# Optimization experiments

Measured on AMD Instinct MI355X. Metric: run time of the kernel, lower is better.

## Reference

```python
import jax, jax.numpy as jnp
import numpy as np

H = 128          # hidden_size
B = 64           # batch of users
T = 20           # current-session length (== max_sess_len)
S = 10           # friend sessions per user (graph degree)
L = 20           # max_sess_len
NUM_ITEMS = 50000
NUM_USERS = 10000
TOPK = 2         # topk in sess_similarity


def gru(x, W_ih, W_hh, b_ih, b_hh):
    """torch nn.GRU (1 layer, batch_first). x: [N, T, H] -> outputs [N, T, H], h_T [N, H]."""
    h0 = jnp.zeros((x.shape[0], x.shape[-1]), x.dtype)

    def step(h, xt):
        gi = xt @ W_ih.T + b_ih          # [N, 3H]
        gh = h @ W_hh.T + b_hh
        i_r, i_z, i_n = jnp.split(gi, 3, axis=-1)
        h_r, h_z, h_n = jnp.split(gh, 3, axis=-1)
        r = jax.nn.sigmoid(i_r + h_r)
        z = jax.nn.sigmoid(i_z + h_z)
        n = jnp.tanh(i_n + r * h_n)
        h = (1.0 - z) * n + z * h
        return h, h

    hT, ys = jax.lax.scan(step, h0, jnp.swapaxes(x, 0, 1))
    return jnp.swapaxes(ys, 0, 1), hT


def masked_softmax(x, mask, axis):
    neg = jnp.finfo(x.dtype).min
    return jax.nn.softmax(jnp.where(mask, x, neg), axis=axis)


def setup_inputs() -> dict:
    key = jax.random.key(0)
    ks = jax.random.split(key, 12)
    users = jax.random.randint(ks[0], (B,), 0, NUM_USERS)
    cur_sess = jax.random.randint(ks[1], (B, T), 0, NUM_ITEMS)          # all valid -> full length
    hist_sess = jax.random.randint(ks[2], (B, S, L), 0, NUM_ITEMS)
    frds_sess = jax.random.randint(ks[3], (B, S, L), 0, NUM_ITEMS)
    cur_sess_len = jnp.full((B,), T, dtype=jnp.int32)
    # parameters
    v_emb = jax.random.uniform(ks[4], (NUM_ITEMS + 1, H), minval=-1.0, maxval=1.0)
    v_emb = v_emb.at[NUM_ITEMS].set(0.0)                                 # padding_idx row
    u_emb = jax.random.normal(ks[5], (NUM_USERS, H)) * (1.0 / np.sqrt(H))
    sc = 1.0 / np.sqrt(H)
    W_ih = jax.random.normal(ks[6], (3 * H, H)) * sc
    W_hh = jax.random.normal(ks[7], (3 * H, H)) * sc
    b_ih = jnp.zeros((3 * H,), jnp.float32)
    b_hh = jnp.zeros((3 * H,), jnp.float32)
    out1_w = jax.random.normal(ks[8], (NUM_ITEMS, 3 * H)) * (1.0 / np.sqrt(3 * H))
    out1_b = jnp.zeros((NUM_ITEMS,), jnp.float32)
    return dict(users=users, cur_sess=cur_sess, hist_sess=hist_sess, frds_sess=frds_sess,
                cur_sess_len=cur_sess_len, v_emb=v_emb, u_emb=u_emb,
                W_ih=W_ih, W_hh=W_hh, b_ih=b_ih, b_hh=b_hh, out1_w=out1_w, out1_b=out1_b)


def reference(users, cur_sess, hist_sess, frds_sess, cur_sess_len,
              v_emb, u_emb, W_ih, W_hh, b_ih, b_hh, out1_w, out1_b):
    # --- rnn_encoder on current session (dropout p=0, eval) ---
    hs, _ = gru(v_emb[cur_sess], W_ih, W_hh, b_ih, b_hh)                 # [B, T, H]
    query = hs

    # --- friend branch (hist branch is dead: hu is overwritten with zeros) ---
    # sess_encoder: GRU over each friend session's items
    frd_items = v_emb[frds_sess]                                         # [B, S, L, H]
    enc, _ = gru(frd_items.reshape(B * S, L, H), W_ih, W_hh, b_ih, b_hh)
    enc = enc.reshape(B, S, L, H)                                        # encoder_output

    # sess_similarity: max over session positions, softmax over degree (S)
    scores = jnp.einsum('bth,bslh->bstl', query, enc)                    # [B, S, T, L]
    sim_raw = scores.max(axis=-1)                                        # [B, S, T]
    sim1 = jax.nn.softmax(sim_raw, axis=1)
    # preserve: edges that are top-2 most similar for ANY step t (S > TOPK branch)
    _, idx = jax.lax.top_k(jnp.swapaxes(sim1, 1, 2), TOPK)               # [B, T, 2]
    preserve = jax.nn.one_hot(idx, S, dtype=jnp.float32).sum((1, 2)) > 0 # [B, S]

    # sess_embedding_attn on the filtered subgraph (masking == filtering here)
    user_e = u_emb[users]                                                # [B, H]
    w = jax.nn.softmax(jnp.einsum('bh,bslh->bsl', user_e, frd_items), axis=2)
    sess_emb = jnp.einsum('bsl,bslh->bsh', w, frd_items)                 # [B, S, H]

    # user_sess_reduce_func: sim1 (pre-filter softmax values), then two softmaxes
    # over the surviving edges (masked softmax over S)
    m = preserve[:, :, None]                                             # [B, S, 1]
    s = masked_softmax(sim1, m, axis=1)
    s = masked_softmax(s, m, axis=1)
    s = jnp.where(m, s, 0.0)
    hf = jnp.einsum('bst,bsh->bth', s, sess_emb)                         # [B, T, H]

    hu = jnp.zeros_like(hs)                                              # hu = zeros_like(hs)
    output = jnp.concatenate([hs, hu, hf], axis=-1)                      # [B, T, 3H]
    logits = output @ out1_w.T + out1_b                                  # [B, T, NUM_ITEMS]
    return logits
```

## Files before the change

kernel.cpp:

```cpp
#include <hip/hip_runtime.h>
#include <cstdint>
#include <cstddef>

#define H_      128
#define B_      64
#define T_      20
#define S_      10
#define L_      20
#define NITEMS  50000
#define NSEQ    704
#define NTOK    (NSEQ * 20)
#define NPAD    50048
#define KA      256

typedef __attribute__((ext_vector_type(8))) short short8;
typedef __attribute__((ext_vector_type(4))) float f32x4;

__device__ __forceinline__ unsigned short f2bf(float f) {
  unsigned int u = __float_as_uint(f);
  u += 0x7FFF + ((u >> 16) & 1);
  return (unsigned short)(u >> 16);
}
__device__ __forceinline__ float sigmoidf_(float x) {
  return 1.0f / (1.0f + __expf(-x));
}

__global__ void __launch_bounds__(256) k1_convert_w(const float* __restrict__ w,
                                                    unsigned short* __restrict__ wb) {
  int t = blockIdx.x * 256 + threadIdx.x;
  int n = t >> 5, kc = t & 31;
  int k0 = kc * 8;
  unsigned int o0, o1, o2, o3;
  if (n < NITEMS) {
    int src = (k0 < 128) ? k0 : (k0 + 128);
    const float* p = w + (size_t)n * 384 + src;
    float4 f0 = *(const float4*)p;
    float4 f1 = *(const float4*)(p + 4);
    o0 = (unsigned)f2bf(f0.x) | ((unsigned)f2bf(f0.y) << 16);
    o1 = (unsigned)f2bf(f0.z) | ((unsigned)f2bf(f0.w) << 16);
    o2 = (unsigned)f2bf(f1.x) | ((unsigned)f2bf(f1.y) << 16);
    o3 = (unsigned)f2bf(f1.z) | ((unsigned)f2bf(f1.w) << 16);
  } else {
    o0 = o1 = o2 = o3 = 0u;
  }
  *(uint4*)(wb + (size_t)n * 256 + k0) = make_uint4(o0, o1, o2, o3);
}

__global__ void __launch_bounds__(384) k2_gi(const int* __restrict__ cur,
                                             const int* __restrict__ frd,
                                             const float* __restrict__ vemb,
                                             const float* __restrict__ Wih,
                                             const float* __restrict__ bih,
                                             float* __restrict__ gi) {
  __shared__ float xs[16 * 128];
  __shared__ int ids[16];
  int tid = threadIdx.x;
  int tok0 = blockIdx.x * 16;
  if (tid < 16) {
    int tok = tok0 + tid;
    int seq = tok / 20, tt = tok % 20;
    ids[tid] = (seq < 64) ? cur[seq * 20 + tt] : frd[(seq - 64) * 20 + tt];
  }
  __syncthreads();
  for (int idx = tid; idx < 512; idx += 384) {
    int i = idx >> 5, kc = idx & 31;
    *(float4*)&xs[i * 128 + kc * 4] =
        *(const float4*)&vemb[(size_t)ids[i] * 128 + kc * 4];
  }
  __syncthreads();
  int j  = tid % 192;
  int th = tid / 192;
  float acc0[8], acc1[8];
#pragma unroll
  for (int i = 0; i < 8; i++) { acc0[i] = 0.f; acc1[i] = 0.f; }
  const float* wr0 = Wih + (size_t)j * 128;
  const float* wr1 = Wih + (size_t)(j + 192) * 128;
  const float* xb = &xs[th * 8 * 128];
  for (int kc = 0; kc < 32; kc++) {
    float4 wa = *(const float4*)(wr0 + kc * 4);
    float4 wc = *(const float4*)(wr1 + kc * 4);
#pragma unroll
    for (int i = 0; i < 8; i++) {
      float4 x4 = *(const float4*)&xb[i * 128 + kc * 4];
      acc0[i] += wa.x * x4.x + wa.y * x4.y + wa.z * x4.z + wa.w * x4.w;
      acc1[i] += wc.x * x4.x + wc.y * x4.y + wc.z * x4.z + wc.w * x4.w;
    }
  }
  float ba = bih[j], bc = bih[j + 192];
#pragma unroll
  for (int i = 0; i < 8; i++) {
    size_t row = (size_t)(tok0 + th * 8 + i) * 384;
    gi[row + j]       = acc0[i] + ba;
    gi[row + j + 192] = acc1[i] + bc;
  }
}

__global__ void __launch_bounds__(384) k3_gru(const float* __restrict__ Whh,
                                              const float* __restrict__ bhh,
                                              const float* __restrict__ gi,
                                              float* __restrict__ out_h) {
  __shared__ float hb[3 * 128];
  __shared__ float pre[3 * 256];
  __shared__ float gin[3 * 128];
  __shared__ float ghn[3 * 128];
  int j = threadIdx.x;
  int seq0 = blockIdx.x * 3;
  int G = NSEQ - seq0; if (G > 3) G = 3;
  float4 wv[32];
  const float4* wr = (const float4*)(Whh + (size_t)j * 128);
#pragma unroll
  for (int kc = 0; kc < 32; kc++) wv[kc] = wr[kc];
  float bb = bhh[j];
  if (j < 128) { hb[j] = 0.f; hb[128 + j] = 0.f; hb[256 + j] = 0.f; }
  __syncthreads();
  if (G == 3) {
    for (int t = 0; t < 20; t++) {
      float a0 = bb, a1 = bb, a2 = bb;
#pragma unroll
      for (int kc = 0; kc < 32; kc++) {
        float4 w4 = wv[kc];
        float4 h0 = *(const float4*)&hb[0 * 128 + kc * 4];
        float4 h1 = *(const float4*)&hb[1 * 128 + kc * 4];
        float4 h2 = *(const float4*)&hb[2 * 128 + kc * 4];
        a0 += w4.x * h0.x + w4.y * h0.y + w4.z * h0.z + w4.w * h0.w;
        a1 += w4.x * h1.x + w4.y * h1.y + w4.z * h1.z + w4.w * h1.w;
        a2 += w4.x * h2.x + w4.y * h2.y + w4.z * h2.z + w4.w * h2.w;
      }
      float g0 = gi[(size_t)((seq0 + 0) * 20 + t) * 384 + j];
      float g1 = gi[(size_t)((seq0 + 1) * 20 + t) * 384 + j];
      float g2 = gi[(size_t)((seq0 + 2) * 20 + t) * 384 + j];
      if (j < 256) {
        pre[0 * 256 + j] = g0 + a0;
        pre[1 * 256 + j] = g1 + a1;
        pre[2 * 256 + j] = g2 + a2;
      } else {
        gin[0 * 128 + (j - 256)] = g0; ghn[0 * 128 + (j - 256)] = a0;
        gin[1 * 128 + (j - 256)] = g1; ghn[1 * 128 + (j - 256)] = a1;
        gin[2 * 128 + (j - 256)] = g2; ghn[2 * 128 + (j - 256)] = a2;
      }
      __syncthreads();
      if (j < 128) {
#pragma unroll
        for (int g = 0; g < 3; g++) {
          float r = sigmoidf_(pre[g * 256 + j]);
          float z = sigmoidf_(pre[g * 256 + 128 + j]);
          float n = tanhf(gin[g * 128 + j] + r * ghn[g * 128 + j]);
          float hN = (1.f - z) * n + z * hb[g * 128 + j];
          hb[g * 128 + j] = hN;
          out_h[(size_t)((seq0 + g) * 20 + t) * 128 + j] = hN;
        }
      }
      __syncthreads();
    }
  } else {
    for (int t = 0; t < 20; t++) {
      for (int g = 0; g < G; g++) {
        float acc = bb;
#pragma unroll
        for (int kc = 0; kc < 32; kc++) {
          float4 h4 = *(const float4*)&hb[g * 128 + kc * 4];
          float4 w4 = wv[kc];
          acc += w4.x * h4.x + w4.y * h4.y + w4.z * h4.z + w4.w * h4.w;
        }
        float gv = gi[(size_t)((seq0 + g) * 20 + t) * 384 + j];
        if (j < 256) pre[g * 256 + j] = gv + acc;
        else { gin[g * 128 + (j - 256)] = gv; ghn[g * 128 + (j - 256)] = acc; }
      }
      __syncthreads();
      if (j < 128) {
        for (int g = 0; g < G; g++) {
          float r = sigmoidf_(pre[g * 256 + j]);
          float z = sigmoidf_(pre[g * 256 + 128 + j]);
          float n = tanhf(gin[g * 128 + j] + r * ghn[g * 128 + j]);
          float hN = (1.f - z) * n + z * hb[g * 128 + j];
          hb[g * 128 + j] = hN;
          out_h[(size_t)((seq0 + g) * 20 + t) * 128 + j] = hN;
        }
      }
      __syncthreads();
    }
  }
}

__global__ void __launch_bounds__(256) k46(const int* __restrict__ users,
                                           const int* __restrict__ frd,
                                           const float* __restrict__ vemb,
                                           const float* __restrict__ uemb,
                                           const float* __restrict__ out_h,
                                           float* __restrict__ sim_raw,
                                           float* __restrict__ sess) {
  __shared__ float qs[20 * 132];
  __shared__ float es[20 * 132];
  __shared__ float fs[20 * 132];
  __shared__ float sc[400];
  __shared__ float us[128];
  __shared__ float dt[20];
  __shared__ float wl[20];
  __shared__ int fid[20];
  int tid = threadIdx.x;
  int b = blockIdx.x / 10, s = blockIdx.x % 10;
  int eseq = 64 + b * 10 + s;
  if (tid < 20) fid[tid] = frd[(size_t)(b * 10 + s) * 20 + tid];
  if (tid < 128) us[tid] = uemb[(size_t)users[b] * 128 + tid];
  __syncthreads();
  for (int idx = tid; idx < 640; idx += 256) {
    int row = idx >> 5, kc = idx & 31;
    *(float4*)&fs[row * 132 + kc * 4] =
        *(const float4*)&vemb[(size_t)fid[row] * 128 + kc * 4];
    *(float4*)&qs[row * 132 + kc * 4] =
        *(const float4*)&out_h[(size_t)(b * 20 + row) * 128 + kc * 4];
    *(float4*)&es[row * 132 + kc * 4] =
        *(const float4*)&out_h[(size_t)(eseq * 20 + row) * 128 + kc * 4];
  }
  __syncthreads();
  for (int idx = tid; idx < 400; idx += 256) {
    int t = idx / 20, l = idx % 20;
    float acc = 0.f;
#pragma unroll
    for (int kc = 0; kc < 32; kc++) {
      float4 q4 = *(const float4*)&qs[t * 132 + kc * 4];
      float4 e4 = *(const float4*)&es[l * 132 + kc * 4];
      acc += q4.x * e4.x + q4.y * e4.y + q4.z * e4.z + q4.w * e4.w;
    }
    sc[idx] = acc;
  }
  if (tid < 20) {
    float acc = 0.f;
    for (int kc = 0; kc < 32; kc++) {
      float4 u4 = *(const float4*)&us[kc * 4];
      float4 f4 = *(const float4*)&fs[tid * 132 + kc * 4];
      acc += u4.x * f4.x + u4.y * f4.y + u4.z * f4.z + u4.w * f4.w;
    }
    dt[tid] = acc;
  }
  __syncthreads();
  if (tid < 20) {
    float m = sc[tid * 20];
    for (int l = 1; l < 20; l++) m = fmaxf(m, sc[tid * 20 + l]);
    sim_raw[(size_t)(b * 10 + s) * 20 + tid] = m;
    float mx = -3.4e38f;
    for (int l = 0; l < 20; l++) mx = fmaxf(mx, dt[l]);
    float sum = 0.f;
    for (int l = 0; l < 20; l++) sum += __expf(dt[l] - mx);
    wl[tid] = __expf(dt[tid] - mx) / sum;
  }
  __syncthreads();
  if (tid < 128) {
    float acc = 0.f;
    for (int l = 0; l < 20; l++) acc += wl[l] * fs[l * 132 + tid];
    sess[(size_t)(b * 10 + s) * 128 + tid] = acc;
  }
}

__global__ void __launch_bounds__(256) k5_fused(const float* __restrict__ sim_raw,
                                                const float* __restrict__ sess,
                                                const float* __restrict__ out_h,
                                                unsigned int* __restrict__ act) {
  __shared__ float sv[200];
  __shared__ float s1[200];
  __shared__ float sf[200];
  __shared__ float se[10 * 128];
  __shared__ int pres[10];
  int tid = threadIdx.x;
  int b = blockIdx.x;
  for (int idx = tid; idx < 200; idx += 256) sv[idx] = sim_raw[(size_t)b * 200 + idx];
  for (int idx = tid; idx < 1280; idx += 256) se[idx] = sess[(size_t)b * 1280 + idx];
  if (tid < 10) pres[tid] = 0;
  __syncthreads();
  if (tid < 20) {
    int t = tid;
    float mx = -3.4e38f;
    for (int s = 0; s < 10; s++) mx = fmaxf(mx, sv[s * 20 + t]);
    float sum = 0.f;
    for (int s = 0; s < 10; s++) sum += __expf(sv[s * 20 + t] - mx);
    float inv = 1.0f / sum;
    float v1 = -1.f, v2 = -1.f; int i1 = 0, i2 = 0;
    for (int s = 0; s < 10; s++) {
      float v = __expf(sv[s * 20 + t] - mx) * inv;
      s1[s * 20 + t] = v;
      if (v > v1) { v2 = v1; i2 = i1; v1 = v; i1 = s; }
      else if (v > v2) { v2 = v; i2 = s; }
    }
    atomicOr(&pres[i1], 1);
    atomicOr(&pres[i2], 1);
  }
  __syncthreads();
  if (tid < 20) {
    int t = tid;
    float mx = -3.4e38f;
    for (int s = 0; s < 10; s++) if (pres[s]) mx = fmaxf(mx, s1[s * 20 + t]);
    float sum = 0.f;
    for (int s = 0; s < 10; s++) if (pres[s]) sum += __expf(s1[s * 20 + t] - mx);
    float inv = 1.f / sum;
    float mx2 = -3.4e38f;
    for (int s = 0; s < 10; s++)
      if (pres[s]) mx2 = fmaxf(mx2, __expf(s1[s * 20 + t] - mx) * inv);
    float sum2 = 0.f;
    for (int s = 0; s < 10; s++)
      if (pres[s]) sum2 += __expf(__expf(s1[s * 20 + t] - mx) * inv - mx2);
    float inv2 = 1.f / sum2;
    for (int s = 0; s < 10; s++) {
      float o = 0.f;
      if (pres[s]) o = __expf(__expf(s1[s * 20 + t] - mx) * inv - mx2) * inv2;
      sf[s * 20 + t] = o;
    }
  }
  __syncthreads();
  for (int idx = tid; idx < 2560; idx += 256) {
    int t = idx >> 7, p = idx & 127;
    int m = b * 20 + t;
    float a0, a1;
    if (p < 64) {
      a0 = out_h[(size_t)m * 128 + p * 2];
      a1 = out_h[(size_t)m * 128 + p * 2 + 1];
    } else {
      int h0 = (p - 64) * 2;
      float acc0 = 0.f, acc1 = 0.f;
#pragma unroll
      for (int s = 0; s < 10; s++) {
        float w = sf[s * 20 + t];
        acc0 += w * se[s * 128 + h0];
        acc1 += w * se[s * 128 + h0 + 1];
      }
      a0 = acc0; a1 = acc1;
    }
    act[(size_t)m * 128 + p] = (unsigned)f2bf(a0) | ((unsigned)f2bf(a1) << 16);
  }
}

__device__ __forceinline__ void async_cp16(const unsigned short* g, unsigned short* l) {
  __builtin_amdgcn_global_load_lds((__attribute__((address_space(1))) void*)g,
                                   (__attribute__((address_space(3))) void*)l,
                                   16, 0, 0);
}

__global__ void __launch_bounds__(256) k9_gemm(const unsigned short* __restrict__ act,
                                               const unsigned short* __restrict__ wb,
                                               const float* __restrict__ bias,
                                               float* __restrict__ out) {
  __shared__ __align__(16) unsigned short Bs[128 * 256];
  __shared__ __align__(16) unsigned short As[128 * 40];
  int tid = threadIdx.x;
  int w = tid >> 6, lane = tid & 63;
  int q = (lane >> 4) & 3, c = lane & 15;
  int wm = w >> 1, wn = w & 1;
  int nb0 = blockIdx.x * 128;

#pragma unroll
  for (int i = 0; i < 16; i++) {
    int n_l = i * 8 + w * 2 + (lane >> 5);
    int p = lane & 31;
    int kc = p ^ (n_l & 31);
    async_cp16(wb + (size_t)(nb0 + n_l) * 256 + kc * 8,
               &Bs[(i * 8 + w * 2) * 256]);
  }

  float bs[4]; int okn[4]; int ncol[4];
#pragma unroll
  for (int nt = 0; nt < 4; nt++) {
    int n = nb0 + wn * 64 + nt * 16 + c;
    ncol[nt] = n;
    okn[nt] = (n < NITEMS);
    bs[nt] = (n < NITEMS) ? bias[n] : 0.f;
  }

  for (int mc = 0; mc < 10; mc++) {
    f32x4 acc[4][4];
#pragma unroll
    for (int mt = 0; mt < 4; mt++)
#pragma unroll
      for (int nt = 0; nt < 4; nt++) {
        f32x4 z = {0.f, 0.f, 0.f, 0.f};
        acc[mt][nt] = z;
      }
    for (int kf = 0; kf < 8; kf++) {
      __syncthreads();
      {
        int ch0 = tid * 2;
#pragma unroll
        for (int jj = 0; jj < 2; jj++) {
          int ch = ch0 + jj;
          int row = ch >> 2, kk = ch & 3;
          short8 v = *(const short8*)&act[(size_t)(mc * 128 + row) * 256 + kf * 32 + kk * 8];
          *(short8*)&As[row * 40 + kk * 8] = v;
        }
      }
      __syncthreads();
      short8 bfr[4];
#pragma unroll
      for (int nt = 0; nt < 4; nt++) {
        int n_l = wn * 64 + nt * 16 + c;
        int slot = n_l * 32 + ((kf * 4 + q) ^ (n_l & 31));
        bfr[nt] = *(const short8*)&Bs[slot * 8];
      }
#pragma unroll
      for (int mt = 0; mt < 4; mt++) {
        int row = wm * 64 + mt * 16 + c;
        short8 af = *(const short8*)&As[row * 40 + q * 8];
#pragma unroll
        for (int nt = 0; nt < 4; nt++)
          acc[mt][nt] = __builtin_amdgcn_mfma_f32_16x16x32_bf16(af, bfr[nt], acc[mt][nt], 0, 0, 0);
      }
    }
#pragma unroll
    for (int nt = 0; nt < 4; nt++) {
      if (okn[nt]) {
#pragma unroll
        for (int mt = 0; mt < 4; mt++) {
          int m = mc * 128 + wm * 64 + mt * 16 + q * 4;
#pragma unroll
          for (int r = 0; r < 4; r++)
            out[(size_t)(m + r) * NITEMS + ncol[nt]] = acc[mt][nt][r] + bs[nt];
        }
      }
    }
  }
}

extern "C" void kernel_launch(void* const* d_in, const int* in_sizes, int n_in,
                              void* d_out, int out_size, void* d_ws, size_t ws_size,
                              hipStream_t stream) {
  const int*   users = (const int*)d_in[0];
  const int*   cur   = (const int*)d_in[1];
  const int*   frd   = (const int*)d_in[3];
  const float* vemb  = (const float*)d_in[5];
  const float* uemb  = (const float*)d_in[6];
  const float* Wih   = (const float*)d_in[7];
  const float* Whh   = (const float*)d_in[8];
  const float* bih   = (const float*)d_in[9];
  const float* bhh   = (const float*)d_in[10];
  const float* w1    = (const float*)d_in[11];
  const float* b1    = (const float*)d_in[12];
  float* out = (float*)d_out;

  char* ws = (char*)d_ws;
  size_t off = 0;
  auto alloc = [&](size_t bytes) -> void* {
    void* p = ws + off;
    off = (off + bytes + 255) & ~(size_t)255;
    return p;
  };
  unsigned short* wb   = (unsigned short*)alloc((size_t)NPAD * 256 * 2);
  unsigned int*   act  = (unsigned int*)alloc((size_t)1280 * 128 * 4);
  float*          gi   = (float*)alloc((size_t)NTOK * 384 * 4);
  float*          outh = (float*)alloc((size_t)NTOK * 128 * 4);
  float*          simr = (float*)alloc((size_t)12800 * 4);
  float*          sess = (float*)alloc((size_t)640 * 128 * 4);

  k1_convert_w<<<NPAD / 8, 256, 0, stream>>>(w1, wb);
  k2_gi<<<NTOK / 16, 384, 0, stream>>>(cur, frd, vemb, Wih, bih, gi);
  k3_gru<<<(NSEQ + 2) / 3, 384, 0, stream>>>(Whh, bhh, gi, outh);
  k46<<<640, 256, 0, stream>>>(users, frd, vemb, uemb, outh, simr, sess);
  k5_fused<<<64, 256, 0, stream>>>(simr, sess, outh, (unsigned int*)act);
  k9_gemm<<<NPAD / 128, 256, 0, stream>>>((const unsigned short*)act, wb, b1, out);
}
```

Baseline: 531.5 us.

## Merge weight conversion with input gates, fuse attention tail, split GEMM over M

Runs the bf16 weight conversion and the GRU input-gate projection as one launch, using a block-index split. The per-user similarity/softmax kernel is folded into the friend-session kernel through an atomic counter, so the last block for each user finishes the reduction. The output GEMM grid is doubled so that each block covers half of the M rows, which raises parallelism but reloads each B tile twice. Together these cut launch overhead and the serialization between small kernels, at the cost of added atomics and threadfences.

```diff
diff --git a/kernel.cpp b/kernel.cpp
--- a/kernel.cpp
+++ b/kernel.cpp
@@ -12,6 +12,8 @@
 #define NTOK    (NSEQ * 20)
 #define NPAD    50048
 #define KA      256
+#define K2BLOCKS 880
+#define K1BLOCKS 4171
 
 typedef __attribute__((ext_vector_type(8))) short short8;
 typedef __attribute__((ext_vector_type(4))) float f32x4;
@@ -25,73 +27,78 @@
   return 1.0f / (1.0f + __expf(-x));
 }
 
-__global__ void __launch_bounds__(256) k1_convert_w(const float* __restrict__ w,
-                                                    unsigned short* __restrict__ wb) {
-  int t = blockIdx.x * 256 + threadIdx.x;
-  int n = t >> 5, kc = t & 31;
-  int k0 = kc * 8;
-  unsigned int o0, o1, o2, o3;
-  if (n < NITEMS) {
-    int src = (k0 < 128) ? k0 : (k0 + 128);
-    const float* p = w + (size_t)n * 384 + src;
-    float4 f0 = *(const float4*)p;
-    float4 f1 = *(const float4*)(p + 4);
-    o0 = (unsigned)f2bf(f0.x) | ((unsigned)f2bf(f0.y) << 16);
-    o1 = (unsigned)f2bf(f0.z) | ((unsigned)f2bf(f0.w) << 16);
-    o2 = (unsigned)f2bf(f1.x) | ((unsigned)f2bf(f1.y) << 16);
-    o3 = (unsigned)f2bf(f1.z) | ((unsigned)f2bf(f1.w) << 16);
+__global__ void __launch_bounds__(384) k12(const float* __restrict__ w,
+                                           unsigned short* __restrict__ wb,
+                                           const int* __restrict__ cur,
+                                           const int* __restrict__ frd,
+                                           const float* __restrict__ vemb,
+                                           const float* __restrict__ Wih,
+                                           const float* __restrict__ bih,
+                                           float* __restrict__ gi,
+                                           int* __restrict__ cnt) {
+  int tid = threadIdx.x;
+  if (blockIdx.x < K2BLOCKS) {
+    __shared__ float xs[16 * 128];
+    __shared__ int ids[16];
+    if (blockIdx.x == 0 && tid < 64) cnt[tid] = 0;
+    int tok0 = blockIdx.x * 16;
+    if (tid < 16) {
+      int tok = tok0 + tid;
+      int seq = tok / 20, tt = tok % 20;
+      ids[tid] = (seq < 64) ? cur[seq * 20 + tt] : frd[(seq - 64) * 20 + tt];
+    }
+    __syncthreads();
+    for (int idx = tid; idx < 512; idx += 384) {
+      int i = idx >> 5, kc = idx & 31;
+      *(float4*)&xs[i * 128 + kc * 4] =
+          *(const float4*)&vemb[(size_t)ids[i] * 128 + kc * 4];
+    }
+    __syncthreads();
+    int j  = tid % 192;
+    int th = tid / 192;
+    float acc0[8], acc1[8];
+#pragma unroll
+    for (int i = 0; i < 8; i++) { acc0[i] = 0.f; acc1[i] = 0.f; }
+    const float* wr0 = Wih + (size_t)j * 128;
+    const float* wr1 = Wih + (size_t)(j + 192) * 128;
+    const float* xb = &xs[th * 8 * 128];
+    for (int kc = 0; kc < 32; kc++) {
+      float4 wa = *(const float4*)(wr0 + kc * 4);
+      float4 wc = *(const float4*)(wr1 + kc * 4);
+#pragma unroll
+      for (int i = 0; i < 8; i++) {
+        float4 x4 = *(const float4*)&xb[i * 128 + kc * 4];
+        acc0[i] += wa.x * x4.x + wa.y * x4.y + wa.z * x4.z + wa.w * x4.w;
+        acc1[i] += wc.x * x4.x + wc.y * x4.y + wc.z * x4.z + wc.w * x4.w;
+      }
+    }
+    float ba = bih[j], bc = bih[j + 192];
+#pragma unroll
+    for (int i = 0; i < 8; i++) {
+      size_t row = (size_t)(tok0 + th * 8 + i) * 384;
+      gi[row + j]       = acc0[i] + ba;
+      gi[row + j + 192] = acc1[i] + bc;
+    }
   } else {
-    o0 = o1 = o2 = o3 = 0u;
-  }
-  *(uint4*)(wb + (size_t)n * 256 + k0) = make_uint4(o0, o1, o2, o3);
-}
-
-__global__ void __launch_bounds__(384) k2_gi(const int* __restrict__ cur,
-                                             const int* __restrict__ frd,
-                                             const float* __restrict__ vemb,
-                                             const float* __restrict__ Wih,
-                                             const float* __restrict__ bih,
-                                             float* __restrict__ gi) {
-  __shared__ float xs[16 * 128];
-  __shared__ int ids[16];
-  int tid = threadIdx.x;
-  int tok0 = blockIdx.x * 16;
-  if (tid < 16) {
-    int tok = tok0 + tid;
-    int seq = tok / 20, tt = tok % 20;
-    ids[tid] = (seq < 64) ? cur[seq * 20 + tt] : frd[(seq - 64) * 20 + tt];
-  }
-  __syncthreads();
-  for (int idx = tid; idx < 512; idx += 384) {
-    int i = idx >> 5, kc = idx & 31;
-    *(float4*)&xs[i * 128 + kc * 4] =
-        *(const float4*)&vemb[(size_t)ids[i] * 128 + kc * 4];
-  }
-  __syncthreads();
-  int j  = tid % 192;
-  int th = tid / 192;
-  float acc0[8], acc1[8];
-#pragma unroll
-  for (int i = 0; i < 8; i++) { acc0[i] = 0.f; acc1[i] = 0.f; }
-  const float* wr0 = Wih + (size_t)j * 128;
-  const float* wr1 = Wih + (size_t)(j + 192) * 128;
-  const float* xb = &xs[th * 8 * 128];
-  for (int kc = 0; kc < 32; kc++) {
-    float4 wa = *(const float4*)(wr0 + kc * 4);
-    float4 wc = *(const float4*)(wr1 + kc * 4);
-#pragma unroll
-    for (int i = 0; i < 8; i++) {
-      float4 x4 = *(const float4*)&xb[i * 128 + kc * 4];
-      acc0[i] += wa.x * x4.x + wa.y * x4.y + wa.z * x4.z + wa.w * x4.w;
-      acc1[i] += wc.x * x4.x + wc.y * x4.y + wc.z * x4.z + wc.w * x4.w;
-    }
-  }
-  float ba = bih[j], bc = bih[j + 192];
-#pragma unroll
-  for (int i = 0; i < 8; i++) {
-    size_t row = (size_t)(tok0 + th * 8 + i) * 384;
-    gi[row + j]       = acc0[i] + ba;
-    gi[row + j + 192] = acc1[i] + bc;
+    int t = (blockIdx.x - K2BLOCKS) * 384 + tid;
+    if (t < NPAD * 32) {
+      int n = t >> 5, kc = t & 31;
+      int k0 = kc * 8;
+      unsigned int o0, o1, o2, o3;
+      if (n < NITEMS) {
+        int src = (k0 < 128) ? k0 : (k0 + 128);
+        const float* p = w + (size_t)n * 384 + src;
+        float4 f0 = *(const float4*)p;
+        float4 f1 = *(const float4*)(p + 4);
+        o0 = (unsigned)f2bf(f0.x) | ((unsigned)f2bf(f0.y) << 16);
+        o1 = (unsigned)f2bf(f0.z) | ((unsigned)f2bf(f0.w) << 16);
+        o2 = (unsigned)f2bf(f1.x) | ((unsigned)f2bf(f1.y) << 16);
+        o3 = (unsigned)f2bf(f1.z) | ((unsigned)f2bf(f1.w) << 16);
+      } else {
+        o0 = o1 = o2 = o3 = 0u;
+      }
+      *(uint4*)(wb + (size_t)n * 256 + k0) = make_uint4(o0, o1, o2, o3);
+    }
   }
 }
 
@@ -182,13 +189,15 @@
   }
 }
 
-__global__ void __launch_bounds__(256) k46(const int* __restrict__ users,
-                                           const int* __restrict__ frd,
-                                           const float* __restrict__ vemb,
-                                           const float* __restrict__ uemb,
-                                           const float* __restrict__ out_h,
-                                           float* __restrict__ sim_raw,
-                                           float* __restrict__ sess) {
+__global__ void __launch_bounds__(256) k46f(const int* __restrict__ users,
+                                            const int* __restrict__ frd,
+                                            const float* __restrict__ vemb,
+                                            const float* __restrict__ uemb,
+                                            const float* __restrict__ out_h,
+                                            float* __restrict__ sim_raw,
+                                            float* __restrict__ sess,
+                                            int* __restrict__ cnt,
+                                            unsigned int* __restrict__ act) {
   __shared__ float qs[20 * 132];
   __shared__ float es[20 * 132];
   __shared__ float fs[20 * 132];
@@ -197,6 +206,7 @@
   __shared__ float dt[20];
   __shared__ float wl[20];
   __shared__ int fid[20];
+  __shared__ int lastflag;
   int tid = threadIdx.x;
   int b = blockIdx.x / 10, s = blockIdx.x % 10;
   int eseq = 64 + b * 10 + s;
@@ -250,19 +260,18 @@
     for (int l = 0; l < 20; l++) acc += wl[l] * fs[l * 132 + tid];
     sess[(size_t)(b * 10 + s) * 128 + tid] = acc;
   }
-}
-
-__global__ void __launch_bounds__(256) k5_fused(const float* __restrict__ sim_raw,
-                                                const float* __restrict__ sess,
-                                                const float* __restrict__ out_h,
-                                                unsigned int* __restrict__ act) {
-  __shared__ float sv[200];
-  __shared__ float s1[200];
-  __shared__ float sf[200];
-  __shared__ float se[10 * 128];
-  __shared__ int pres[10];
-  int tid = threadIdx.x;
-  int b = blockIdx.x;
+  __syncthreads();
+  __threadfence();
+  if (tid == 0) lastflag = (atomicAdd(&cnt[b], 1) == 9);
+  __syncthreads();
+  if (!lastflag) return;
+  __threadfence();
+
+  float* sv = sc;
+  float* s1 = qs;
+  float* sf = qs + 400;
+  float* se = es;
+  int* pres = fid;
   for (int idx = tid; idx < 200; idx += 256) sv[idx] = sim_raw[(size_t)b * 200 + idx];
   for (int idx = tid; idx < 1280; idx += 256) se[idx] = sess[(size_t)b * 1280 + idx];
   if (tid < 10) pres[tid] = 0;
@@ -270,16 +279,16 @@
   if (tid < 20) {
     int t = tid;
     float mx = -3.4e38f;
-    for (int s = 0; s < 10; s++) mx = fmaxf(mx, sv[s * 20 + t]);
+    for (int ss = 0; ss < 10; ss++) mx = fmaxf(mx, sv[ss * 20 + t]);
     float sum = 0.f;
-    for (int s = 0; s < 10; s++) sum += __expf(sv[s * 20 + t] - mx);
+    for (int ss = 0; ss < 10; ss++) sum += __expf(sv[ss * 20 + t] - mx);
     float inv = 1.0f / sum;
     float v1 = -1.f, v2 = -1.f; int i1 = 0, i2 = 0;
-    for (int s = 0; s < 10; s++) {
-      float v = __expf(sv[s * 20 + t] - mx) * inv;
-      s1[s * 20 + t] = v;
-      if (v > v1) { v2 = v1; i2 = i1; v1 = v; i1 = s; }
-      else if (v > v2) { v2 = v; i2 = s; }
+    for (int ss = 0; ss < 10; ss++) {
+      float v = __expf(sv[ss * 20 + t] - mx) * inv;
+      s1[ss * 20 + t] = v;
+      if (v > v1) { v2 = v1; i2 = i1; v1 = v; i1 = ss; }
+      else if (v > v2) { v2 = v; i2 = ss; }
     }
     atomicOr(&pres[i1], 1);
     atomicOr(&pres[i2], 1);
@@ -288,21 +297,21 @@
   if (tid < 20) {
     int t = tid;
     float mx = -3.4e38f;
-    for (int s = 0; s < 10; s++) if (pres[s]) mx = fmaxf(mx, s1[s * 20 + t]);
+    for (int ss = 0; ss < 10; ss++) if (pres[ss]) mx = fmaxf(mx, s1[ss * 20 + t]);
     float sum = 0.f;
-    for (int s = 0; s < 10; s++) if (pres[s]) sum += __expf(s1[s * 20 + t] - mx);
+    for (int ss = 0; ss < 10; ss++) if (pres[ss]) sum += __expf(s1[ss * 20 + t] - mx);
     float inv = 1.f / sum;
     float mx2 = -3.4e38f;
-    for (int s = 0; s < 10; s++)
-      if (pres[s]) mx2 = fmaxf(mx2, __expf(s1[s * 20 + t] - mx) * inv);
+    for (int ss = 0; ss < 10; ss++)
+      if (pres[ss]) mx2 = fmaxf(mx2, __expf(s1[ss * 20 + t] - mx) * inv);
     float sum2 = 0.f;
-    for (int s = 0; s < 10; s++)
-      if (pres[s]) sum2 += __expf(__expf(s1[s * 20 + t] - mx) * inv - mx2);
+    for (int ss = 0; ss < 10; ss++)
+      if (pres[ss]) sum2 += __expf(__expf(s1[ss * 20 + t] - mx) * inv - mx2);
     float inv2 = 1.f / sum2;
-    for (int s = 0; s < 10; s++) {
+    for (int ss = 0; ss < 10; ss++) {
       float o = 0.f;
-      if (pres[s]) o = __expf(__expf(s1[s * 20 + t] - mx) * inv - mx2) * inv2;
-      sf[s * 20 + t] = o;
+      if (pres[ss]) o = __expf(__expf(s1[ss * 20 + t] - mx) * inv - mx2) * inv2;
+      sf[ss * 20 + t] = o;
     }
   }
   __syncthreads();
@@ -317,10 +326,10 @@
       int h0 = (p - 64) * 2;
       float acc0 = 0.f, acc1 = 0.f;
 #pragma unroll
-      for (int s = 0; s < 10; s++) {
-        float w = sf[s * 20 + t];
-        acc0 += w * se[s * 128 + h0];
-        acc1 += w * se[s * 128 + h0 + 1];
+      for (int ss = 0; ss < 10; ss++) {
+        float w = sf[ss * 20 + t];
+        acc0 += w * se[ss * 128 + h0];
+        acc1 += w * se[ss * 128 + h0 + 1];
       }
       a0 = acc0; a1 = acc1;
     }
@@ -344,7 +353,8 @@
   int w = tid >> 6, lane = tid & 63;
   int q = (lane >> 4) & 3, c = lane & 15;
   int wm = w >> 1, wn = w & 1;
-  int nb0 = blockIdx.x * 128;
+  int tile = blockIdx.x >> 1, mh = blockIdx.x & 1;
+  int nb0 = tile * 128;
 
 #pragma unroll
   for (int i = 0; i < 16; i++) {
@@ -364,7 +374,7 @@
     bs[nt] = (n < NITEMS) ? bias[n] : 0.f;
   }
 
-  for (int mc = 0; mc < 10; mc++) {
+  for (int mc = mh * 5; mc < mh * 5 + 5; mc++) {
     f32x4 acc[4][4];
 #pragma unroll
     for (int mt = 0; mt < 4; mt++)
@@ -446,11 +456,11 @@
   float*          outh = (float*)alloc((size_t)NTOK * 128 * 4);
   float*          simr = (float*)alloc((size_t)12800 * 4);
   float*          sess = (float*)alloc((size_t)640 * 128 * 4);
-
-  k1_convert_w<<<NPAD / 8, 256, 0, stream>>>(w1, wb);
-  k2_gi<<<NTOK / 16, 384, 0, stream>>>(cur, frd, vemb, Wih, bih, gi);
+  int*            cnt  = (int*)alloc(64 * 4);
+
+  k12<<<K2BLOCKS + K1BLOCKS, 384, 0, stream>>>(w1, wb, cur, frd, vemb, Wih, bih, gi, cnt);
   k3_gru<<<(NSEQ + 2) / 3, 384, 0, stream>>>(Whh, bhh, gi, outh);
-  k46<<<640, 256, 0, stream>>>(users, frd, vemb, uemb, outh, simr, sess);
-  k5_fused<<<64, 256, 0, stream>>>(simr, sess, outh, (unsigned int*)act);
-  k9_gemm<<<NPAD / 128, 256, 0, stream>>>((const unsigned short*)act, wb, b1, out);
-}
+  k46f<<<640, 256, 0, stream>>>(users, frd, vemb, uemb, outh, simr, sess, cnt,
+                                (unsigned int*)act);
+  k9_gemm<<<(NPAD / 128) * 2, 256, 0, stream>>>((const unsigned short*)act, wb, b1, out);
+}
```

Result: slower. 590.4 us (+11.1%).
